# Optimization experiments

Hardware: AMD Instinct MI355X
Metric: run time of the kernel (lower is better)

The kernel has to match this reference:

```python
import math
import jax, jax.numpy as jnp
import numpy as np

B, C, H, W = 4, 256, 64, 64
KEEP = 0.1


def setup_inputs() -> dict:
    key = jax.random.key(0)
    kx, kq, kk, kv = jax.random.split(key, 4)
    scale = 1.0 / math.sqrt(C)
    return {
        "x": jax.random.normal(kx, (B, C, H, W), dtype=jnp.float32),
        "Wq": jax.random.normal(kq, (C, C), dtype=jnp.float32) * scale,
        "Wk": jax.random.normal(kk, (C, C), dtype=jnp.float32) * scale,
        "Wv": jax.random.normal(kv, (C, C), dtype=jnp.float32) * scale,
    }


def reference(x, Wq, Wk, Wv):
    b, c, h, w = x.shape
    n = h * w
    xt = x.reshape(b, c, n).transpose(0, 2, 1)          # [B, N, C] tokens
    # 1x1 conv with weight [C_out, C_in] == token-wise linear: tok @ W^T
    q = jnp.einsum('bnc,dc->bnd', xt, Wq)
    k = jnp.einsum('bnc,dc->bnd', xt, Wk)
    v = jnp.einsum('bnc,dc->bnd', xt, Wv)

    scores = jnp.einsum('bqd,bkd->bqk', q, k) / math.sqrt(c)   # [B, N, N]
    k_keep = max(1, int(KEEP * n))
    topk_vals, topk_idx = jax.lax.top_k(scores, k_keep)        # [B, N, k]

    # scatter top-k values into a -inf mask, then softmax over all N keys
    neg_inf = jnp.finfo(scores.dtype).min
    mask = jnp.full_like(scores, neg_inf)
    bi = jnp.arange(b)[:, None, None]
    qi = jnp.arange(n)[None, :, None]
    mask = mask.at[bi, qi, topk_idx].set(topk_vals)
    attn = jax.nn.softmax(mask, axis=-1)                       # [B, N, N]

    out = jnp.einsum('bqk,bkd->bqd', attn, v)                  # [B, N, C]
    return out.transpose(0, 2, 1).reshape(b, c, h, w)
```

## Files before the change

kernel.cpp:

```cpp
#include <hip/hip_runtime.h>
#include <stdint.h>

#define BATCH 4
#define CH    256
#define NTOK  4096
#define KSEL  409

typedef unsigned short u16;
typedef unsigned int   u32;
typedef unsigned long long u64;

typedef __attribute__((ext_vector_type(8))) _Float16 half8;
typedef __attribute__((ext_vector_type(4))) _Float16 half4;
typedef __attribute__((ext_vector_type(4))) float f32x4;
typedef __attribute__((ext_vector_type(4))) u32 u32x4;
typedef __attribute__((ext_vector_type(2))) u32 u32x2;
typedef __attribute__((ext_vector_type(4))) float fl4;

__device__ inline u16 h2u(_Float16 h){ u16 u; __builtin_memcpy(&u,&h,2); return u; }
__device__ inline float u2f16(u32 v){ _Float16 h; u16 uu=(u16)v; __builtin_memcpy(&h,&uu,2); return (float)h; }
__device__ inline float kinv16(u32 k){
  u32 v = (k & 0x8000u) ? (k & 0x7FFFu) : ((~k) & 0xFFFFu);
  return u2f16(v);
}
__device__ inline void gload16(const void* g, void* l){
  __builtin_amdgcn_global_load_lds((const __attribute__((address_space(1))) u32*)g,
                                   (__attribute__((address_space(3))) u32*)l, 16, 0, 0);
}

__global__ __launch_bounds__(256) void wsplit_kernel(
    const float* __restrict__ Wq, const float* __restrict__ Wk,
    const float* __restrict__ Wv, u16* __restrict__ W3h, u16* __restrict__ W3l)
{
  const int p = blockIdx.y;
  const float* W = (p==0)? Wq : (p==1)? Wk : Wv;
  const int idx = (blockIdx.x*256 + threadIdx.x) * 4;
  fl4 v = *(const fl4*)(W + idx);
  u32x2 vh, vl;
  #pragma unroll
  for (int q=0;q<2;q++) {
    _Float16 h0=(_Float16)v[q*2], h1=(_Float16)v[q*2+1];
    _Float16 l0=(_Float16)(v[q*2]-(float)h0), l1=(_Float16)(v[q*2+1]-(float)h1);
    vh[q] = (u32)h2u(h0) | ((u32)h2u(h1)<<16);
    vl[q] = (u32)h2u(l0) | ((u32)h2u(l1)<<16);
  }
  *(u32x2*)(W3h + p*CH*CH + idx) = vh;
  *(u32x2*)(W3l + p*CH*CH + idx) = vl;
}

__global__ __launch_bounds__(256) void xsplit_kernel(
    const float* __restrict__ x, u16* __restrict__ xTh, u16* __restrict__ xTl)
{
  __shared__ float lds[64][65];
  const int tid = threadIdx.x;
  const int n0 = blockIdx.x << 6;
  const int c0 = blockIdx.y << 6;
  const int b  = blockIdx.z;
  const float* xb = x + (size_t)b*CH*NTOK;

  #pragma unroll
  for (int i=0;i<16;i++) {
    int c_l = (tid>>6) + (i<<2);
    int n_l = tid & 63;
    lds[c_l][n_l] = xb[(size_t)(c0+c_l)*NTOK + n0 + n_l];
  }
  __syncthreads();
  u16* oh = xTh + (size_t)b*NTOK*CH;
  u16* ol = xTl + (size_t)b*NTOK*CH;
  #pragma unroll
  for (int i=0;i<16;i++) {
    int n_l = (tid>>6) + (i<<2);
    int c_l = tid & 63;
    float v = lds[c_l][n_l];
    _Float16 h = (_Float16)v;
    _Float16 l = (_Float16)(v - (float)h);
    size_t o = (size_t)(n0+n_l)*CH + c0 + c_l;
    oh[o] = h2u(h);
    ol[o] = h2u(l);
  }
}

__global__ __launch_bounds__(256) void proj_gemm(
    const u16* __restrict__ xTh, const u16* __restrict__ xTl,
    const u16* __restrict__ W3h, const u16* __restrict__ W3l,
    u16* __restrict__ Qh, u16* __restrict__ Kh, u16* __restrict__ Vc)
{
  __shared__ __align__(16) short lds[4*128*64];
  short* lds_ah = lds;
  short* lds_al = lds + 128*64;
  short* lds_bh = lds + 2*128*64;
  short* lds_bl = lds + 3*128*64;

  const int tid  = threadIdx.x;
  const int lane = tid & 63;
  const int wave = tid >> 6;
  const int wm = wave >> 1, wn = wave & 1;
  const int brow = blockIdx.x << 7;
  const int bcol = blockIdx.y << 7;
  const int z = blockIdx.z;
  const int b = z / 3, p = z - 3*b;

  const u16* Agh = xTh + ((size_t)b*NTOK + brow)*CH;
  const u16* Agl = xTl + ((size_t)b*NTOK + brow)*CH;
  const u16* Bgh = W3h + (size_t)p*CH*CH + (size_t)bcol*CH;
  const u16* Bgl = W3l + (size_t)p*CH*CH + (size_t)bcol*CH;

  f32x4 acc[4][4];
  #pragma unroll
  for (int i=0;i<4;i++)
    #pragma unroll
    for (int j=0;j<4;j++) acc[i][j] = (f32x4)0.f;

  const int sr    = tid >> 3;
  const int sslot = tid & 7;

  for (int kt=0; kt<4; kt++) {
    #pragma unroll
    for (int c=0;c<4;c++) {
      int r  = (c<<5) + sr;
      int ss = sslot ^ (r & 7);
      size_t goff = (size_t)r*CH + (kt<<6) + (ss<<3);
      int dst = (c<<12) + (wave<<10);
      gload16(Agh + goff, (char*)lds_ah + dst);
      gload16(Agl + goff, (char*)lds_al + dst);
      gload16(Bgh + goff, (char*)lds_bh + dst);
      gload16(Bgl + goff, (char*)lds_bl + dst);
    }
    __syncthreads();
    #pragma unroll
    for (int ks=0;ks<2;ks++) {
      half8 ah[4], al[4], bh[4], bl[4];
      const int kg = lane >> 4;
      const int rl = lane & 15;
      #pragma unroll
      for (int t=0;t<4;t++) {
        int ar = (wm<<6) + (t<<4) + rl;
        int slot = (ks<<2) + kg;
        int ao = ar*64 + ((slot ^ (ar&7))<<3);
        ah[t] = *(const half8*)&lds_ah[ao];
        al[t] = *(const half8*)&lds_al[ao];
        int br = (wn<<6) + (t<<4) + rl;
        int bo = br*64 + ((slot ^ (br&7))<<3);
        bh[t] = *(const half8*)&lds_bh[bo];
        bl[t] = *(const half8*)&lds_bl[bo];
      }
      #pragma unroll
      for (int mt=0;mt<4;mt++)
        #pragma unroll
        for (int nt=0;nt<4;nt++) {
          acc[mt][nt] = __builtin_amdgcn_mfma_f32_16x16x32_f16(ah[mt], bh[nt], acc[mt][nt], 0,0,0);
          acc[mt][nt] = __builtin_amdgcn_mfma_f32_16x16x32_f16(ah[mt], bl[nt], acc[mt][nt], 0,0,0);
          acc[mt][nt] = __builtin_amdgcn_mfma_f32_16x16x32_f16(al[mt], bh[nt], acc[mt][nt], 0,0,0);
        }
    }
    __syncthreads();
  }

  const int rl = lane & 15, rg = lane >> 4;
  if (p < 2) {
    u16* oh = ((p==0)? Qh : Kh) + (size_t)b*NTOK*CH;
    #pragma unroll
    for (int mt=0;mt<4;mt++) {
      #pragma unroll
      for (int nt=0;nt<4;nt++) {
        int n = brow + (wm<<6) + (mt<<4) + (rg<<2);
        int c = bcol + (wn<<6) + (nt<<4) + rl;
        #pragma unroll
        for (int r=0;r<4;r++)
          oh[(size_t)(n+r)*CH + c] = h2u((_Float16)acc[mt][nt][r]);
      }
    }
  } else {
    u16* ldsT = (u16*)lds;
    #pragma unroll
    for (int mt=0;mt<4;mt++) {
      #pragma unroll
      for (int nt=0;nt<4;nt++) {
        int n_l = (wm<<6) + (mt<<4) + (rg<<2);
        int c_l = (wn<<6) + (nt<<4) + rl;
        half4 hv;
        #pragma unroll
        for (int r=0;r<4;r++) hv[r] = (_Float16)acc[mt][nt][r];
        *(half4*)&ldsT[c_l*136 + n_l] = hv;
      }
    }
    __syncthreads();
    u16* ov = Vc + (size_t)b*CH*NTOK + (size_t)bcol*NTOK + brow;
    #pragma unroll
    for (int i=0;i<32;i++) {
      int d_l = (tid>>6) + (i<<2);
      u32 v = *(const u32*)&ldsT[d_l*136 + (lane<<1)];
      *(u32*)(ov + (size_t)d_l*NTOK + (lane<<1)) = v;
    }
  }
}

#define WAITV(S)  asm volatile("s_waitcnt " S ::: "memory")
#define RBAR()    __builtin_amdgcn_s_barrier()
#define SCHED0()  __builtin_amdgcn_sched_barrier(0)

#define STAGE_SC(LA, LB, KT)                                                  \
  {                                                                           \
    _Pragma("unroll")                                                         \
    for (int c=0;c<4;c++) {                                                   \
      int r  = (c<<5) + sr;                                                   \
      int ss = sslot ^ (r & 7);                                               \
      size_t goff = (size_t)r*CH + ((KT)<<6) + (ss<<3);                       \
      gload16(Ag + goff, (char*)(LA) + (c<<12) + (wave<<10));                 \
      gload16(Bg + goff, (char*)(LB) + (c<<12) + (wave<<10));                 \
    }                                                                         \
  }

#define COMP_SC(LA, LB)                                                       \
  {                                                                           \
    _Pragma("unroll")                                                         \
    for (int ks=0;ks<2;ks++) {                                                \
      half8 af[4], bf[4];                                                     \
      const int kg = lane >> 4;                                               \
      const int rl = lane & 15;                                               \
      _Pragma("unroll")                                                       \
      for (int t=0;t<4;t++) {                                                 \
        int ar = (wm<<6) + (t<<4) + rl;                                       \
        int slot = (ks<<2) + kg;                                              \
        af[t] = *(const half8*)&(LA)[ar*64 + ((slot ^ (ar&7))<<3)];           \
        int br = (wn<<6) + (t<<4) + rl;                                       \
        bf[t] = *(const half8*)&(LB)[br*64 + ((slot ^ (br&7))<<3)];           \
      }                                                                       \
      _Pragma("unroll")                                                       \
      for (int mt=0;mt<4;mt++)                                                \
        _Pragma("unroll")                                                     \
        for (int nt=0;nt<4;nt++)                                              \
          acc[mt][nt] = __builtin_amdgcn_mfma_f32_16x16x32_f16(af[mt], bf[nt], acc[mt][nt], 0,0,0); \
    }                                                                         \
  }

__global__ __launch_bounds__(256) void score_kernel(
    const u16* __restrict__ Qh, const u16* __restrict__ Kh,
    u16* __restrict__ S, int b)
{
  __shared__ __align__(16) short lds_a0[128*64];
  __shared__ __align__(16) short lds_a1[128*64];
  __shared__ __align__(16) short lds_b0[128*64];
  __shared__ __align__(16) short lds_b1[128*64];
  const int tid  = threadIdx.x;
  const int lane = tid & 63;
  const int wave = tid >> 6;
  const int wm = wave >> 1, wn = wave & 1;
  const int brow = blockIdx.x << 7, bcol = blockIdx.y << 7;

  const u16* Ag = Qh + ((size_t)b*NTOK + brow)*CH;
  const u16* Bg = Kh + ((size_t)b*NTOK + bcol)*CH;

  f32x4 acc[4][4];
  #pragma unroll
  for (int i=0;i<4;i++)
    #pragma unroll
    for (int j=0;j<4;j++) acc[i][j] = (f32x4)0.f;

  const int sr    = tid >> 3;
  const int sslot = tid & 7;

  STAGE_SC(lds_a0, lds_b0, 0);
  STAGE_SC(lds_a1, lds_b1, 1);
  WAITV("vmcnt(8)"); RBAR(); SCHED0();
  COMP_SC(lds_a0, lds_b0);
  RBAR(); SCHED0();
  STAGE_SC(lds_a0, lds_b0, 2);
  WAITV("vmcnt(8)"); RBAR(); SCHED0();
  COMP_SC(lds_a1, lds_b1);
  RBAR(); SCHED0();
  STAGE_SC(lds_a1, lds_b1, 3);
  WAITV("vmcnt(8)"); RBAR(); SCHED0();
  COMP_SC(lds_a0, lds_b0);
  RBAR(); SCHED0();
  WAITV("vmcnt(0)"); RBAR(); SCHED0();
  COMP_SC(lds_a1, lds_b1);

  const int rl = lane & 15, rg = lane >> 4;
  #pragma unroll
  for (int mt=0;mt<4;mt++) {
    #pragma unroll
    for (int nt=0;nt<4;nt++) {
      int row = brow + (wm<<6) + (mt<<4) + (rg<<2);
      int col = bcol + (wn<<6) + (nt<<4) + rl;
      #pragma unroll
      for (int r=0;r<4;r++)
        S[(size_t)(row+r)*NTOK + col] = h2u((_Float16)(acc[mt][nt][r] * 0.0625f));
    }
  }
}

__global__ __launch_bounds__(256) void select_kernel(
    const u16* __restrict__ Sh, u16* __restrict__ Wd)
{
  __shared__ __align__(16) u32 hist[4][256];
  const int lane = threadIdx.x & 63;
  const int wave = threadIdx.x >> 6;
  const int row  = (blockIdx.x << 2) + wave;
  const u16* Srow = Sh + (size_t)row * NTOK + (lane << 3);

  u32 key[64];
  u32 umax = 0;
  #pragma unroll
  for (int g=0; g<8; ++g) {
    u32x4 q = *(const u32x4*)(Srow + (g<<9));
    #pragma unroll
    for (int j=0; j<4; ++j) {
      u32 w = q[j];
      u32 a = w & 0xFFFFu, bb = w >> 16;
      a  = (a  & 0x8000u) ? ((~a)  & 0xFFFFu) : (a  | 0x8000u);
      bb = (bb & 0x8000u) ? ((~bb) & 0xFFFFu) : (bb | 0x8000u);
      key[(g<<3)+(j<<1)  ] = a;
      key[(g<<3)+(j<<1)+1] = bb;
      umax = umax > a  ? umax : a;
      umax = umax > bb ? umax : bb;
    }
  }
  #pragma unroll
  for (int off=32; off; off>>=1) { u32 o = __shfl_xor(umax, off, 64); umax = o>umax ? o : umax; }
  const float m = kinv16(umax);

  u32 krem = KSEL, prefix = 0, cb = 0;
  #pragma unroll
  for (int pass=0; pass<2; ++pass) {
    const int shift = 8 - (pass<<3);
    #pragma unroll
    for (int i=0;i<4;i++) hist[wave][(i<<6)+lane] = 0u;
    __asm__ volatile("s_waitcnt lgkmcnt(0)" ::: "memory");
    if (pass == 0) {
      #pragma unroll
      for (int ch=0; ch<64; ch++) atomicAdd(&hist[wave][key[ch] >> 8], 1u);
    } else {
      const u32 b1 = prefix >> 8;
      #pragma unroll
      for (int ch=0; ch<64; ch++)
        if ((key[ch] >> 8) == b1) atomicAdd(&hist[wave][key[ch] & 255u], 1u);
    }
    __asm__ volatile("s_waitcnt lgkmcnt(0)" ::: "memory");
    u32x4 h = *(const u32x4*)&hist[wave][lane<<2];
    u32 tot = h[0]+h[1]+h[2]+h[3];
    u32 sfx = tot;
    #pragma unroll
    for (int off=1; off<64; off<<=1) {
      u32 v = __shfl_down(sfx, off, 64);
      if (lane + off < 64) sfx += v;
    }
    u32 s3 = (sfx - tot) + h[3];
    u32 s2 = s3 + h[2];
    u32 s1 = s2 + h[1];
    u32 s0 = s1 + h[0];
    u32 s4 = s3 - h[3];
    u32 kr = krem;
    u32 enc = 0;
    if (s0 >= kr && s1 < kr) enc = ((u32)((lane<<2)+0)<<22) | (h[0]<<9) | (kr - s1);
    if (s1 >= kr && s2 < kr) enc = ((u32)((lane<<2)+1)<<22) | (h[1]<<9) | (kr - s2);
    if (s2 >= kr && s3 < kr) enc = ((u32)((lane<<2)+2)<<22) | (h[2]<<9) | (kr - s3);
    if (s3 >= kr && s4 < kr) enc = ((u32)((lane<<2)+3)<<22) | (h[3]<<9) | (kr - s4);
    #pragma unroll
    for (int off=32; off; off>>=1) { u32 o = __shfl_xor(enc, off, 64); enc = (o>enc)? o:enc; }
    prefix |= (enc >> 22) << shift;
    cb      = (enc >> 9) & 0x1FFFu;
    krem    = enc & 0x1FFu;
  }
  const u32 tkey = prefix;

  u64 selb = 0;
  if (cb == krem) {
    #pragma unroll
    for (int ch=0; ch<64; ch++)
      if (key[ch] >= tkey) selb |= (1ull << ch);
  } else {
    const u64 ltmask = (1ull << lane) - 1ull;
    int eqbase = 0;
    #pragma unroll
    for (int ch=0; ch<64; ch++) {
      bool eq = (key[ch] == tkey);
      u64 eqm = __ballot(eq);
      bool sel = (key[ch] > tkey) || (eq && (eqbase + __popcll(eqm & ltmask)) < (int)krem);
      if (sel) selb |= (1ull << ch);
      eqbase += __popcll(eqm);
    }
  }

  float z = 0.f;
  #pragma unroll
  for (int ch=0; ch<64; ch++) {
    float e = __expf(kinv16(key[ch]) - m);
    if ((selb >> ch) & 1ull) z += e;
    key[ch] = __float_as_uint(e);
  }
  #pragma unroll
  for (int off=32; off; off>>=1) z += __shfl_xor(z, off, 64);
  const float invZ = 1.f / z;

  u16* wp = Wd + (size_t)row * NTOK + (lane << 3);
  #pragma unroll
  for (int g=0; g<8; ++g) {
    u32x4 v;
    #pragma unroll
    for (int j=0; j<4; ++j) {
      int i0 = (g<<3)+(j<<1), i1 = i0+1;
      float w0 = ((selb >> i0) & 1ull) ? __uint_as_float(key[i0]) * invZ : 0.f;
      float w1 = ((selb >> i1) & 1ull) ? __uint_as_float(key[i1]) * invZ : 0.f;
      v[j] = (u32)h2u((_Float16)w0) | ((u32)h2u((_Float16)w1) << 16);
    }
    *(u32x4*)(wp + (g<<9)) = v;
  }
}

#define STAGE_PV(LA, LB, KT)                                                  \
  {                                                                           \
    _Pragma("unroll")                                                         \
    for (int c=0;c<4;c++) {                                                   \
      int r  = (c<<5) + sr;                                                   \
      int ss = sslot ^ (r & 7);                                               \
      gload16(Ag + (size_t)r*NTOK + ((KT)<<6) + (ss<<3),                      \
              (char*)(LA) + (c<<12) + (wave<<10));                            \
    }                                                                         \
    _Pragma("unroll")                                                         \
    for (int c=0;c<2;c++) {                                                   \
      int r  = (c<<5) + sr;                                                   \
      int ss = sslot ^ (r & 7);                                               \
      gload16(Bg + (size_t)r*NTOK + ((KT)<<6) + (ss<<3),                      \
              (char*)(LB) + (c<<12) + (wave<<10));                            \
    }                                                                         \
  }

#define COMP_PV(LA, LB)                                                       \
  {                                                                           \
    _Pragma("unroll")                                                         \
    for (int ks=0;ks<2;ks++) {                                                \
      half8 af[4], bf[2];                                                     \
      const int kg = lane >> 4;                                               \
      const int rl = lane & 15;                                               \
      const int slot = (ks<<2) + kg;                                          \
      _Pragma("unroll")                                                       \
      for (int t=0;t<4;t++) {                                                 \
        int ar = (wm<<6) + (t<<4) + rl;                                       \
        af[t] = *(const half8*)&(LA)[ar*64 + ((slot ^ (ar&7))<<3)];           \
      }                                                                       \
      _Pragma("unroll")                                                       \
      for (int t=0;t<2;t++) {                                                 \
        int br = (wn<<5) + (t<<4) + rl;                                       \
        bf[t] = *(const half8*)&(LB)[br*64 + ((slot ^ (br&7))<<3)];           \
      }                                                                       \
      _Pragma("unroll")                                                       \
      for (int mt=0;mt<4;mt++)                                                \
        _Pragma("unroll")                                                     \
        for (int nt=0;nt<2;nt++)                                              \
          acc[mt][nt] = __builtin_amdgcn_mfma_f32_16x16x32_f16(af[mt], bf[nt], acc[mt][nt], 0,0,0); \
    }                                                                         \
  }

#define PV_ITER(LA, LB, VM, TS)                                               \
  WAITV(VM); RBAR(); SCHED0();                                                \
  COMP_PV(LA, LB);                                                            \
  RBAR(); SCHED0();                                                           \
  if ((TS) < 64) STAGE_PV(LA, LB, TS);

__global__ __launch_bounds__(256) void pv_gemm(
    const u16* __restrict__ Vc, const u16* __restrict__ Wd,
    float* __restrict__ out, int b_base, size_t wstride)
{
  __shared__ __align__(16) short lds_a0[128*64];
  __shared__ __align__(16) short lds_a1[128*64];
  __shared__ __align__(16) short lds_b0[64*64];
  __shared__ __align__(16) short lds_b1[64*64];
  const int tid  = threadIdx.x;
  const int lane = tid & 63;
  const int wave = tid >> 6;
  const int wm = wave >> 1, wn = wave & 1;
  const int b    = b_base + blockIdx.z;
  const int brow = blockIdx.x << 7;
  const int bcol = blockIdx.y << 6;

  const u16* Ag = Vc + (size_t)b*CH*NTOK + (size_t)brow*NTOK;
  const u16* Bg = Wd + (size_t)blockIdx.z*wstride + (size_t)bcol*NTOK;

  f32x4 acc[4][2];
  #pragma unroll
  for (int i=0;i<4;i++)
    #pragma unroll
    for (int j=0;j<2;j++) acc[i][j] = (f32x4)0.f;

  const int sr    = tid >> 3;
  const int sslot = tid & 7;

  STAGE_PV(lds_a0, lds_b0, 0);
  STAGE_PV(lds_a1, lds_b1, 1);

  for (int g=0; g<31; ++g) {
    const int t = g*2;
    PV_ITER(lds_a0, lds_b0, "vmcnt(6)", t+2);
    PV_ITER(lds_a1, lds_b1, "vmcnt(6)", t+3);
  }
  WAITV("vmcnt(6)"); RBAR(); SCHED0();
  COMP_PV(lds_a0, lds_b0);
  RBAR(); SCHED0();
  WAITV("vmcnt(0)"); RBAR(); SCHED0();
  COMP_PV(lds_a1, lds_b1);

  float* ob = out + (size_t)b*CH*NTOK;
  const int rl = lane & 15, rg = lane >> 4;
  #pragma unroll
  for (int mt=0;mt<4;mt++) {
    #pragma unroll
    for (int nt=0;nt<2;nt++) {
      int row = brow + (wm<<6) + (mt<<4) + (rg<<2);
      int col = bcol + (wn<<5) + (nt<<4) + rl;
      #pragma unroll
      for (int r=0;r<4;r++)
        ob[(size_t)(row+r)*NTOK + col] = acc[mt][nt][r];
    }
  }
}

extern "C" void kernel_launch(void* const* d_in, const int* in_sizes, int n_in,
                              void* d_out, int out_size, void* d_ws, size_t ws_size,
                              hipStream_t stream)
{
  (void)in_sizes; (void)n_in; (void)out_size;
  const float* x  = (const float*)d_in[0];
  const float* Wq = (const float*)d_in[1];
  const float* Wk = (const float*)d_in[2];
  const float* Wv = (const float*)d_in[3];
  float* out = (float*)d_out;

  char* ws = (char*)d_ws;
  size_t off = 0;
  const size_t plane = (size_t)BATCH*NTOK*CH*2;
  const size_t NN    = (size_t)NTOK*NTOK;
  u16* Qh = (u16*)(ws + off); off += plane;
  u16* Kh = (u16*)(ws + off); off += plane;
  u16* Vc = (u16*)(ws + off); off += plane;
  u16* W3h = (u16*)(ws + off); off += (size_t)3*CH*CH*2;
  u16* W3l = (u16*)(ws + off); off += (size_t)3*CH*CH*2;
  const size_t xt_base = off;
  u16* xTh = (u16*)(ws + xt_base);
  u16* xTl = (u16*)(ws + xt_base + plane);
  const size_t fullW_need = xt_base + (size_t)BATCH*NN*2 + NN*2;
  const bool fullW = ws_size >= fullW_need;
  u16* Wd = (u16*)(ws + xt_base);
  u16* S  = (u16*)(ws + xt_base + (fullW ? (size_t)BATCH*NN*2 : NN*2));

  wsplit_kernel<<<dim3(64,3), 256, 0, stream>>>(Wq, Wk, Wv, W3h, W3l);
  xsplit_kernel<<<dim3(64,4,4), 256, 0, stream>>>(x, xTh, xTl);
  proj_gemm<<<dim3(32,2,12), 256, 0, stream>>>(xTh, xTl, W3h, W3l, Qh, Kh, Vc);

  if (fullW) {
    for (int b=0; b<BATCH; b++) {
      score_kernel<<<dim3(32,32), 256, 0, stream>>>(Qh, Kh, S, b);
      select_kernel<<<1024, 256, 0, stream>>>(S, Wd + (size_t)b*NN);
    }
    pv_gemm<<<dim3(2,64,4), 256, 0, stream>>>(Vc, Wd, out, 0, NN);
  } else {
    for (int b=0; b<BATCH; b++) {
      score_kernel<<<dim3(32,32), 256, 0, stream>>>(Qh, Kh, S, b);
      select_kernel<<<1024, 256, 0, stream>>>(S, Wd);
      pv_gemm<<<dim3(2,64,1), 256, 0, stream>>>(Vc, Wd, out, b, 0);
    }
  }
}
```

Measured before the change: 284.9 us.

## Write softmax weights in place over scores and batch score/select launches

The select kernel now overwrites the score matrix in place with the normalized top-k weights, so the separate weight buffer is gone. Each row is fully loaded into registers before it is written back, which keeps the in-place update safe. Because less workspace is needed, all four batches fit at once, and the score and select kernels each launch once with a batch grid dimension instead of once per batch. This cuts launch count and gives larger grids, and the smaller footprint may also improve cache locality.

```diff
diff --git a/kernel.cpp b/kernel.cpp
--- a/kernel.cpp
+++ b/kernel.cpp
@@ -236,7 +236,7 @@
 
 __global__ __launch_bounds__(256) void score_kernel(
     const u16* __restrict__ Qh, const u16* __restrict__ Kh,
-    u16* __restrict__ S, int b)
+    u16* __restrict__ S, int b_base, size_t sstride)
 {
   __shared__ __align__(16) short lds_a0[128*64];
   __shared__ __align__(16) short lds_a1[128*64];
@@ -247,6 +247,8 @@
   const int wave = tid >> 6;
   const int wm = wave >> 1, wn = wave & 1;
   const int brow = blockIdx.x << 7, bcol = blockIdx.y << 7;
+  const int b = b_base + blockIdx.z;
+  u16* Sb = S + (size_t)blockIdx.z * sstride;
 
   const u16* Ag = Qh + ((size_t)b*NTOK + brow)*CH;
   const u16* Bg = Kh + ((size_t)b*NTOK + bcol)*CH;
@@ -285,19 +287,18 @@
       int col = bcol + (wn<<6) + (nt<<4) + rl;
       #pragma unroll
       for (int r=0;r<4;r++)
-        S[(size_t)(row+r)*NTOK + col] = h2u((_Float16)(acc[mt][nt][r] * 0.0625f));
-    }
-  }
-}
-
-__global__ __launch_bounds__(256) void select_kernel(
-    const u16* __restrict__ Sh, u16* __restrict__ Wd)
+        Sb[(size_t)(row+r)*NTOK + col] = h2u((_Float16)(acc[mt][nt][r] * 0.0625f));
+    }
+  }
+}
+
+__global__ __launch_bounds__(256) void select_kernel(u16* Sh, size_t sstride)
 {
   __shared__ __align__(16) u32 hist[4][256];
   const int lane = threadIdx.x & 63;
   const int wave = threadIdx.x >> 6;
   const int row  = (blockIdx.x << 2) + wave;
-  const u16* Srow = Sh + (size_t)row * NTOK + (lane << 3);
+  u16* Srow = Sh + (size_t)blockIdx.y * sstride + (size_t)row * NTOK + (lane << 3);
 
   u32 key[64];
   u32 umax = 0;
@@ -393,7 +394,6 @@
   for (int off=32; off; off>>=1) z += __shfl_xor(z, off, 64);
   const float invZ = 1.f / z;
 
-  u16* wp = Wd + (size_t)row * NTOK + (lane << 3);
   #pragma unroll
   for (int g=0; g<8; ++g) {
     u32x4 v;
@@ -404,7 +404,7 @@
       float w1 = ((selb >> i1) & 1ull) ? __uint_as_float(key[i1]) * invZ : 0.f;
       v[j] = (u32)h2u((_Float16)w0) | ((u32)h2u((_Float16)w1) << 16);
     }
-    *(u32x4*)(wp + (g<<9)) = v;
+    *(u32x4*)(Srow + (g<<9)) = v;
   }
 }
 
@@ -538,26 +538,23 @@
   const size_t xt_base = off;
   u16* xTh = (u16*)(ws + xt_base);
   u16* xTl = (u16*)(ws + xt_base + plane);
-  const size_t fullW_need = xt_base + (size_t)BATCH*NN*2 + NN*2;
-  const bool fullW = ws_size >= fullW_need;
-  u16* Wd = (u16*)(ws + xt_base);
-  u16* S  = (u16*)(ws + xt_base + (fullW ? (size_t)BATCH*NN*2 : NN*2));
+  u16* S   = (u16*)(ws + xt_base);
+  const size_t full_need = xt_base + (size_t)BATCH*NN*2;
+  const bool full = ws_size >= full_need;
 
   wsplit_kernel<<<dim3(64,3), 256, 0, stream>>>(Wq, Wk, Wv, W3h, W3l);
   xsplit_kernel<<<dim3(64,4,4), 256, 0, stream>>>(x, xTh, xTl);
   proj_gemm<<<dim3(32,2,12), 256, 0, stream>>>(xTh, xTl, W3h, W3l, Qh, Kh, Vc);
 
-  if (fullW) {
-    for (int b=0; b<BATCH; b++) {
-      score_kernel<<<dim3(32,32), 256, 0, stream>>>(Qh, Kh, S, b);
-      select_kernel<<<1024, 256, 0, stream>>>(S, Wd + (size_t)b*NN);
-    }
-    pv_gemm<<<dim3(2,64,4), 256, 0, stream>>>(Vc, Wd, out, 0, NN);
+  if (full) {
+    score_kernel<<<dim3(32,32,4), 256, 0, stream>>>(Qh, Kh, S, 0, NN);
+    select_kernel<<<dim3(1024,4), 256, 0, stream>>>(S, NN);
+    pv_gemm<<<dim3(2,64,4), 256, 0, stream>>>(Vc, S, out, 0, NN);
   } else {
     for (int b=0; b<BATCH; b++) {
-      score_kernel<<<dim3(32,32), 256, 0, stream>>>(Qh, Kh, S, b);
-      select_kernel<<<1024, 256, 0, stream>>>(S, Wd);
-      pv_gemm<<<dim3(2,64,1), 256, 0, stream>>>(Vc, Wd, out, b, 0);
-    }
-  }
-}
+      score_kernel<<<dim3(32,32,1), 256, 0, stream>>>(Qh, Kh, S, b, 0);
+      select_kernel<<<dim3(1024,1), 256, 0, stream>>>(S, 0);
+      pv_gemm<<<dim3(2,64,1), 256, 0, stream>>>(Vc, S, out, b, 0);
+    }
+  }
+}
```

Result: faster. 228.0 us, median of 2 (-20.0%).
